# Optimization experiments

Measured on AMD Instinct MI355X. Metric: run time of the kernel, lower is better.

The kernel has to match this reference:

```python
import jax, jax.numpy as jnp
import numpy as np
from jax import lax

B, N, S, C_IN, C_OUT = 4, 16384, 4096, 256, 256


def setup_inputs() -> dict:
    key = jax.random.key(0)
    k1, k2, k3, k4 = jax.random.split(key, 4)
    xyz1 = jax.random.normal(k1, (B, 3, N), dtype=jnp.float32)
    xyz2 = jax.random.normal(k2, (B, 3, S), dtype=jnp.float32)
    points2 = jax.random.normal(k3, (B, C_IN, S), dtype=jnp.float32)
    W = jax.random.normal(k4, (C_OUT, C_IN), dtype=jnp.float32) * (1.0 / np.sqrt(C_IN))
    b = jnp.zeros((C_OUT,), dtype=jnp.float32)
    return {"xyz1": xyz1, "xyz2": xyz2, "points2": points2, "W": W, "b": b}


def reference(xyz1, xyz2, points2, W, b):
    # channel-first -> channel-last
    p1 = jnp.transpose(xyz1, (0, 2, 1))        # [B, N, 3]
    p2 = jnp.transpose(xyz2, (0, 2, 1))        # [B, S, 3]
    f2 = jnp.transpose(points2, (0, 2, 1))     # [B, S, C]
    Bn, Nn, _ = p1.shape
    Cn = f2.shape[-1]
    # squared pairwise distances [B, N, S]
    d = (-2.0 * jnp.einsum('bnc,bsc->bns', p1, p2)
         + jnp.sum(p1 * p1, axis=-1)[:, :, None]
         + jnp.sum(p2 * p2, axis=-1)[:, None, :])
    # 3 nearest neighbors (smallest distances) -- equivalent to sort + slice :3
    neg_d3, idx = lax.top_k(-d, 3)             # [B, N, 3]
    d3 = -neg_d3
    recip = 1.0 / (d3 + 1e-8)
    weight = recip / jnp.sum(recip, axis=-1, keepdims=True)   # [B, N, 3]
    # gather neighbor features: [B, N, 3, C]
    gathered = jnp.take_along_axis(
        f2, idx.reshape(Bn, Nn * 3)[..., None], axis=1
    ).reshape(Bn, Nn, 3, Cn)
    interp = jnp.sum(gathered * weight[..., None], axis=2)    # [B, N, C]
    # Conv1d(kernel=1) == per-point linear: [B, C_out, N]
    out = jnp.einsum('bnc,oc->bon', interp, W) + b[None, :, None]
    return out
```

## Files before the change

### kernel.cpp

```cpp
#include <hip/hip_runtime.h>

#define BB 4
#define NN 16384
#define SS 4096
#define CIN 256
#define COUT 256

#define SC 8
#define SCS (SS / SC)
#define KNNB ((NN / 512) * SC * BB)
#define GEMMB ((COUT / 64) * (SS / 64) * BB)

__device__ __forceinline__ unsigned short f2bf(float f) {
    unsigned u = __float_as_uint(f);
    u += 0x7FFF + ((u >> 16) & 1);
    return (unsigned short)(u >> 16);
}
__device__ __forceinline__ float bf2f(unsigned short h) {
    return __uint_as_float((unsigned)h << 16);
}

__global__ __launch_bounds__(256) void k_fused(const float* __restrict__ xyz1,
                                               const float* __restrict__ xyz2,
                                               const float* __restrict__ P,
                                               const float* __restrict__ W,
                                               const float* __restrict__ bias,
                                               unsigned short* __restrict__ Gh,
                                               float* __restrict__ pd,
                                               int* __restrict__ pi) {
    __shared__ float smem[2112];
    int bid = blockIdx.x;
    int t   = threadIdx.x;

    if (bid < KNNB) {
        int nb = bid & 31;
        int ch = (bid >> 5) & 7;
        int b  = bid >> 8;
        int s0 = ch * SCS;

        float4* smv = (float4*)smem;
        const float* x2 = xyz2 + (size_t)b * 3 * SS;
        for (int i = t; i < SCS; i += 256) {
            float px = x2[s0 + i];
            float py = x2[SS + s0 + i];
            float pz = x2[2 * SS + s0 + i];
            smv[i] = make_float4(px, py, pz, fmaf(px, px, fmaf(py, py, pz * pz)));
        }
        __syncthreads();

        int n0  = nb * 512 + t;
        int n1q = n0 + 256;
        const float* xb = xyz1 + (size_t)b * 3 * NN;
        float ax = xb[n0],  ay = xb[NN + n0],  az = xb[2 * NN + n0];
        float bx = xb[n1q], by = xb[NN + n1q], bz = xb[2 * NN + n1q];
        float an1 = fmaf(ax, ax, fmaf(ay, ay, az * az));
        float bn1 = fmaf(bx, bx, fmaf(by, by, bz * bz));
        float axm2 = -2.0f * ax, aym2 = -2.0f * ay, azm2 = -2.0f * az;
        float bxm2 = -2.0f * bx, bym2 = -2.0f * by, bzm2 = -2.0f * bz;

        float Ad0 = 3.4e38f, Ad1 = 3.4e38f, Ad2 = 3.4e38f;
        float Bd0 = 3.4e38f, Bd1 = 3.4e38f, Bd2 = 3.4e38f;
        int Ai0 = 0, Ai1 = 0, Ai2 = 0;
        int Bi0 = 0, Bi1 = 0, Bi2 = 0;

#pragma unroll 8
        for (int s = 0; s < SCS; ++s) {
            float4 p = smv[s];
            int gs = s0 + s;
            {
                float d = fmaf(p.x, axm2, fmaf(p.y, aym2,
                          fmaf(p.z, azm2, p.w + an1)));
                bool c0 = d < Ad0, c1 = d < Ad1, c2 = d < Ad2;
                Ad2 = __builtin_amdgcn_fmed3f(Ad1, d, Ad2);
                Ad1 = __builtin_amdgcn_fmed3f(Ad0, d, Ad1);
                Ad0 = fminf(Ad0, d);
                Ai2 = c1 ? Ai1 : (c2 ? gs : Ai2);
                Ai1 = c0 ? Ai0 : (c1 ? gs : Ai1);
                Ai0 = c0 ? gs : Ai0;
            }
            {
                float d = fmaf(p.x, bxm2, fmaf(p.y, bym2,
                          fmaf(p.z, bzm2, p.w + bn1)));
                bool c0 = d < Bd0, c1 = d < Bd1, c2 = d < Bd2;
                Bd2 = __builtin_amdgcn_fmed3f(Bd1, d, Bd2);
                Bd1 = __builtin_amdgcn_fmed3f(Bd0, d, Bd1);
                Bd0 = fminf(Bd0, d);
                Bi2 = c1 ? Bi1 : (c2 ? gs : Bi2);
                Bi1 = c0 ? Bi0 : (c1 ? gs : Bi1);
                Bi0 = c0 ? gs : Bi0;
            }
        }

        size_t cb = (size_t)(ch * BB + b) * 3;
        pd[(cb + 0) * NN + n0]  = Ad0;  pd[(cb + 1) * NN + n0]  = Ad1;
        pd[(cb + 2) * NN + n0]  = Ad2;
        pi[(cb + 0) * NN + n0]  = Ai0;  pi[(cb + 1) * NN + n0]  = Ai1;
        pi[(cb + 2) * NN + n0]  = Ai2;
        pd[(cb + 0) * NN + n1q] = Bd0;  pd[(cb + 1) * NN + n1q] = Bd1;
        pd[(cb + 2) * NN + n1q] = Bd2;
        pi[(cb + 0) * NN + n1q] = Bi0;  pi[(cb + 1) * NN + n1q] = Bi1;
        pi[(cb + 2) * NN + n1q] = Bi2;
    } else {
        int g  = bid - KNNB;
        int o0 = (g & 3) * 64;
        int s0 = ((g >> 2) & 63) * 64;
        int b  = g >> 8;
        float* sP = smem;
        float* sW = smem + 1024;
        int i = t & 15;
        int j = t >> 4;

        float acc[4][4];
#pragma unroll
        for (int p = 0; p < 4; ++p)
#pragma unroll
            for (int q = 0; q < 4; ++q) acc[p][q] = 0.f;

        const float* Pb = P + (size_t)b * CIN * SS;

        for (int c0 = 0; c0 < CIN; c0 += 16) {
            __syncthreads();
            {
                int col = t & 63;
                int r0r = t >> 6;
#pragma unroll
                for (int r = 0; r < 4; ++r) {
                    int row = r0r + r * 4;
                    sP[row * 64 + col] = Pb[(size_t)(c0 + row) * SS + s0 + col];
                }
            }
            {
                int cc = t & 15;
                int obase = t >> 4;
#pragma unroll
                for (int r = 0; r < 4; ++r) {
                    int oo = obase + 16 * r;
                    sW[cc * 68 + oo] = W[(size_t)(o0 + oo) * CIN + c0 + cc];
                }
            }
            __syncthreads();

#pragma unroll
            for (int cc = 0; cc < 16; ++cc) {
                float4 a  = *(const float4*)&sP[cc * 64 + i * 4];
                float4 bv = *(const float4*)&sW[cc * 68 + j * 4];
                float av[4] = {a.x, a.y, a.z, a.w};
                float bw[4] = {bv.x, bv.y, bv.z, bv.w};
#pragma unroll
                for (int p = 0; p < 4; ++p)
#pragma unroll
                    for (int q = 0; q < 4; ++q)
                        acc[p][q] = fmaf(av[p], bw[q], acc[p][q]);
            }
        }

        float b0 = bias[o0 + j * 4 + 0];
        float b1 = bias[o0 + j * 4 + 1];
        float b2 = bias[o0 + j * 4 + 2];
        float b3 = bias[o0 + j * 4 + 3];
#pragma unroll
        for (int p = 0; p < 4; ++p) {
            ushort4 v;
            v.x = f2bf(acc[p][0] + b0);
            v.y = f2bf(acc[p][1] + b1);
            v.z = f2bf(acc[p][2] + b2);
            v.w = f2bf(acc[p][3] + b3);
            size_t off = ((size_t)b * SS + s0 + i * 4 + p) * COUT + o0 + j * 4;
            *(ushort4*)&Gh[off] = v;
        }
    }
}

__global__ __launch_bounds__(256) void k_out(const unsigned short* __restrict__ Gh,
                                             const float* __restrict__ pd,
                                             const int* __restrict__ pi,
                                             float* __restrict__ out) {
    __shared__ float tile[64 * 65];
    __shared__ float ptd[64][12];
    __shared__ int   pti[64][12];
    __shared__ float sw[64][3];
    __shared__ int   si[64][3];
    int b    = blockIdx.y;
    int n0   = blockIdx.x * 64;
    int t    = threadIdx.x;
    int wave = t >> 6;
    int lane = t & 63;

    {
        int n = n0 + lane;
        float d0 = 3.4e38f, d1 = 3.4e38f, d2 = 3.4e38f;
        int i0 = 0, i1 = 0, i2 = 0;
#pragma unroll
        for (int c = 0; c < 2; ++c) {
            size_t cb = (size_t)((wave * 2 + c) * BB + b) * 3;
#pragma unroll
            for (int j = 0; j < 3; ++j) {
                float d = pd[(cb + j) * NN + n];
                int   s = pi[(cb + j) * NN + n];
                bool c0 = d < d0, c1 = d < d1, c2 = d < d2;
                d2 = __builtin_amdgcn_fmed3f(d1, d, d2);
                d1 = __builtin_amdgcn_fmed3f(d0, d, d1);
                d0 = fminf(d0, d);
                i2 = c1 ? i1 : (c2 ? s : i2);
                i1 = c0 ? i0 : (c1 ? s : i1);
                i0 = c0 ? s : i0;
            }
        }
        ptd[lane][wave * 3 + 0] = d0; pti[lane][wave * 3 + 0] = i0;
        ptd[lane][wave * 3 + 1] = d1; pti[lane][wave * 3 + 1] = i1;
        ptd[lane][wave * 3 + 2] = d2; pti[lane][wave * 3 + 2] = i2;
    }
    __syncthreads();
    if (t < 64) {
        float d0 = 3.4e38f, d1 = 3.4e38f, d2 = 3.4e38f;
        int i0 = 0, i1 = 0, i2 = 0;
#pragma unroll
        for (int c = 0; c < 12; ++c) {
            float d = ptd[t][c];
            int   s = pti[t][c];
            bool c0 = d < d0, c1 = d < d1, c2 = d < d2;
            d2 = __builtin_amdgcn_fmed3f(d1, d, d2);
            d1 = __builtin_amdgcn_fmed3f(d0, d, d1);
            d0 = fminf(d0, d);
            i2 = c1 ? i1 : (c2 ? s : i2);
            i1 = c0 ? i0 : (c1 ? s : i1);
            i0 = c0 ? s : i0;
        }
        float r0 = 1.0f / (d0 + 1e-8f);
        float r1 = 1.0f / (d1 + 1e-8f);
        float r2 = 1.0f / (d2 + 1e-8f);
        float inv = 1.0f / (r0 + r1 + r2);
        sw[t][0] = r0 * inv; sw[t][1] = r1 * inv; sw[t][2] = r2 * inv;
        si[t][0] = i0;       si[t][1] = i1;       si[t][2] = i2;
    }
    __syncthreads();

    const unsigned short* Gb = Gh + (size_t)b * SS * COUT;
    float* obase = out + (size_t)b * COUT * NN + n0 + lane;

    for (int oc = 0; oc < 4; ++oc) {
        int o0 = oc * 64;
#pragma unroll 4
        for (int qi = wave; qi < 64; qi += 4) {
            float w0 = sw[qi][0], w1 = sw[qi][1], w2 = sw[qi][2];
            const unsigned short* r0 = Gb + (size_t)si[qi][0] * COUT + o0;
            const unsigned short* r1 = Gb + (size_t)si[qi][1] * COUT + o0;
            const unsigned short* r2 = Gb + (size_t)si[qi][2] * COUT + o0;
            tile[qi * 65 + lane] = fmaf(w0, bf2f(r0[lane]),
                                   fmaf(w1, bf2f(r1[lane]),
                                        w2 * bf2f(r2[lane])));
        }
        __syncthreads();
#pragma unroll
        for (int j = 0; j < 16; ++j) {
            int c = wave * 16 + j;
            obase[(size_t)(o0 + c) * NN] = tile[lane * 65 + c];
        }
        __syncthreads();
    }
}

extern "C" void kernel_launch(void* const* d_in, const int* in_sizes, int n_in,
                              void* d_out, int out_size, void* d_ws, size_t ws_size,
                              hipStream_t stream) {
    const float* xyz1    = (const float*)d_in[0];
    const float* xyz2    = (const float*)d_in[1];
    const float* points2 = (const float*)d_in[2];
    const float* W       = (const float*)d_in[3];
    const float* bias    = (const float*)d_in[4];
    float* out = (float*)d_out;

    char* ws = (char*)d_ws;
    float*          pd = (float*)(ws);
    int*            pi = (int*)(ws + 6291456);
    unsigned short* Gh = (unsigned short*)(ws + 12582912);

    k_fused<<<dim3(KNNB + GEMMB), 256, 0, stream>>>(xyz1, xyz2, points2, W, bias,
                                                    Gh, pd, pi);
    k_out<<<dim3(NN / 64, BB), 256, 0, stream>>>(Gh, pd, pi, out);
}
```

Before: 226.9 us.

## Split top-3 merge into own kernel, vectorize and parallelize gather-output over channels

The per-query norm term is dropped from the inner distance loop and added only when the partial results are stored, removing one add per candidate. The chunk merge and weight computation move into a separate k_merge kernel that writes packed float4 weights and int4 indices. k_out now launches one block per 64-channel slice, so there are four times as many blocks. Each block gathers ushort4 vectors, so fewer, wider loads replace many scalar loads. This trades an extra launch and some workspace traffic for a shorter KNN inner loop and more parallel, vectorized gather/transpose work.

```diff
diff --git a/kernel.cpp b/kernel.cpp
--- a/kernel.cpp
+++ b/kernel.cpp
@@ -68,23 +68,21 @@
             float4 p = smv[s];
             int gs = s0 + s;
             {
-                float d = fmaf(p.x, axm2, fmaf(p.y, aym2,
-                          fmaf(p.z, azm2, p.w + an1)));
-                bool c0 = d < Ad0, c1 = d < Ad1, c2 = d < Ad2;
-                Ad2 = __builtin_amdgcn_fmed3f(Ad1, d, Ad2);
-                Ad1 = __builtin_amdgcn_fmed3f(Ad0, d, Ad1);
-                Ad0 = fminf(Ad0, d);
+                float e = fmaf(p.x, axm2, fmaf(p.y, aym2, fmaf(p.z, azm2, p.w)));
+                bool c0 = e < Ad0, c1 = e < Ad1, c2 = e < Ad2;
+                Ad2 = __builtin_amdgcn_fmed3f(Ad1, e, Ad2);
+                Ad1 = __builtin_amdgcn_fmed3f(Ad0, e, Ad1);
+                Ad0 = fminf(Ad0, e);
                 Ai2 = c1 ? Ai1 : (c2 ? gs : Ai2);
                 Ai1 = c0 ? Ai0 : (c1 ? gs : Ai1);
                 Ai0 = c0 ? gs : Ai0;
             }
             {
-                float d = fmaf(p.x, bxm2, fmaf(p.y, bym2,
-                          fmaf(p.z, bzm2, p.w + bn1)));
-                bool c0 = d < Bd0, c1 = d < Bd1, c2 = d < Bd2;
-                Bd2 = __builtin_amdgcn_fmed3f(Bd1, d, Bd2);
-                Bd1 = __builtin_amdgcn_fmed3f(Bd0, d, Bd1);
-                Bd0 = fminf(Bd0, d);
+                float e = fmaf(p.x, bxm2, fmaf(p.y, bym2, fmaf(p.z, bzm2, p.w)));
+                bool c0 = e < Bd0, c1 = e < Bd1, c2 = e < Bd2;
+                Bd2 = __builtin_amdgcn_fmed3f(Bd1, e, Bd2);
+                Bd1 = __builtin_amdgcn_fmed3f(Bd0, e, Bd1);
+                Bd0 = fminf(Bd0, e);
                 Bi2 = c1 ? Bi1 : (c2 ? gs : Bi2);
                 Bi1 = c0 ? Bi0 : (c1 ? gs : Bi1);
                 Bi0 = c0 ? gs : Bi0;
@@ -92,12 +90,12 @@
         }
 
         size_t cb = (size_t)(ch * BB + b) * 3;
-        pd[(cb + 0) * NN + n0]  = Ad0;  pd[(cb + 1) * NN + n0]  = Ad1;
-        pd[(cb + 2) * NN + n0]  = Ad2;
+        pd[(cb + 0) * NN + n0]  = Ad0 + an1;  pd[(cb + 1) * NN + n0]  = Ad1 + an1;
+        pd[(cb + 2) * NN + n0]  = Ad2 + an1;
         pi[(cb + 0) * NN + n0]  = Ai0;  pi[(cb + 1) * NN + n0]  = Ai1;
         pi[(cb + 2) * NN + n0]  = Ai2;
-        pd[(cb + 0) * NN + n1q] = Bd0;  pd[(cb + 1) * NN + n1q] = Bd1;
-        pd[(cb + 2) * NN + n1q] = Bd2;
+        pd[(cb + 0) * NN + n1q] = Bd0 + bn1;  pd[(cb + 1) * NN + n1q] = Bd1 + bn1;
+        pd[(cb + 2) * NN + n1q] = Bd2 + bn1;
         pi[(cb + 0) * NN + n1q] = Bi0;  pi[(cb + 1) * NN + n1q] = Bi1;
         pi[(cb + 2) * NN + n1q] = Bi2;
     } else {
@@ -171,53 +169,22 @@
     }
 }
 
-__global__ __launch_bounds__(256) void k_out(const unsigned short* __restrict__ Gh,
-                                             const float* __restrict__ pd,
-                                             const int* __restrict__ pi,
-                                             float* __restrict__ out) {
-    __shared__ float tile[64 * 65];
-    __shared__ float ptd[64][12];
-    __shared__ int   pti[64][12];
-    __shared__ float sw[64][3];
-    __shared__ int   si[64][3];
-    int b    = blockIdx.y;
-    int n0   = blockIdx.x * 64;
-    int t    = threadIdx.x;
-    int wave = t >> 6;
-    int lane = t & 63;
-
-    {
-        int n = n0 + lane;
-        float d0 = 3.4e38f, d1 = 3.4e38f, d2 = 3.4e38f;
-        int i0 = 0, i1 = 0, i2 = 0;
-#pragma unroll
-        for (int c = 0; c < 2; ++c) {
-            size_t cb = (size_t)((wave * 2 + c) * BB + b) * 3;
-#pragma unroll
-            for (int j = 0; j < 3; ++j) {
-                float d = pd[(cb + j) * NN + n];
-                int   s = pi[(cb + j) * NN + n];
-                bool c0 = d < d0, c1 = d < d1, c2 = d < d2;
-                d2 = __builtin_amdgcn_fmed3f(d1, d, d2);
-                d1 = __builtin_amdgcn_fmed3f(d0, d, d1);
-                d0 = fminf(d0, d);
-                i2 = c1 ? i1 : (c2 ? s : i2);
-                i1 = c0 ? i0 : (c1 ? s : i1);
-                i0 = c0 ? s : i0;
-            }
-        }
-        ptd[lane][wave * 3 + 0] = d0; pti[lane][wave * 3 + 0] = i0;
-        ptd[lane][wave * 3 + 1] = d1; pti[lane][wave * 3 + 1] = i1;
-        ptd[lane][wave * 3 + 2] = d2; pti[lane][wave * 3 + 2] = i2;
-    }
-    __syncthreads();
-    if (t < 64) {
-        float d0 = 3.4e38f, d1 = 3.4e38f, d2 = 3.4e38f;
-        int i0 = 0, i1 = 0, i2 = 0;
-#pragma unroll
-        for (int c = 0; c < 12; ++c) {
-            float d = ptd[t][c];
-            int   s = pti[t][c];
+__global__ __launch_bounds__(256) void k_merge(const float* __restrict__ pd,
+                                               const int* __restrict__ pi,
+                                               float4* __restrict__ wi4,
+                                               int4* __restrict__ gi4) {
+    int b = blockIdx.y;
+    int n = blockIdx.x * 256 + threadIdx.x;
+
+    float d0 = 3.4e38f, d1 = 3.4e38f, d2 = 3.4e38f;
+    int i0 = 0, i1 = 0, i2 = 0;
+#pragma unroll
+    for (int ch = 0; ch < SC; ++ch) {
+        size_t cb = (size_t)(ch * BB + b) * 3;
+#pragma unroll
+        for (int j = 0; j < 3; ++j) {
+            float d = pd[(cb + j) * NN + n];
+            int   s = pi[(cb + j) * NN + n];
             bool c0 = d < d0, c1 = d < d1, c2 = d < d2;
             d2 = __builtin_amdgcn_fmed3f(d1, d, d2);
             d1 = __builtin_amdgcn_fmed3f(d0, d, d1);
@@ -226,37 +193,70 @@
             i1 = c0 ? i0 : (c1 ? s : i1);
             i0 = c0 ? s : i0;
         }
-        float r0 = 1.0f / (d0 + 1e-8f);
-        float r1 = 1.0f / (d1 + 1e-8f);
-        float r2 = 1.0f / (d2 + 1e-8f);
-        float inv = 1.0f / (r0 + r1 + r2);
-        sw[t][0] = r0 * inv; sw[t][1] = r1 * inv; sw[t][2] = r2 * inv;
-        si[t][0] = i0;       si[t][1] = i1;       si[t][2] = i2;
+    }
+
+    float r0 = 1.0f / (d0 + 1e-8f);
+    float r1 = 1.0f / (d1 + 1e-8f);
+    float r2 = 1.0f / (d2 + 1e-8f);
+    float inv = 1.0f / (r0 + r1 + r2);
+    size_t q = (size_t)b * NN + n;
+    wi4[q] = make_float4(r0 * inv, r1 * inv, r2 * inv, 0.f);
+    gi4[q] = make_int4(i0, i1, i2, 0);
+}
+
+__global__ __launch_bounds__(256) void k_out(const unsigned short* __restrict__ Gh,
+                                             const float4* __restrict__ wi4,
+                                             const int4* __restrict__ gi4,
+                                             float* __restrict__ out) {
+    __shared__ float  tile[64 * 68];
+    __shared__ float4 swv[64];
+    __shared__ int4   siv[64];
+    int b    = blockIdx.z;
+    int oc   = blockIdx.y;
+    int n0   = blockIdx.x * 64;
+    int o0   = oc * 64;
+    int t    = threadIdx.x;
+    int wave = t >> 6;
+    int lane = t & 63;
+    int qg   = lane >> 4;
+    int c16  = lane & 15;
+
+    if (t < 64) {
+        size_t q = (size_t)b * NN + n0 + t;
+        swv[t] = wi4[q];
+        siv[t] = gi4[q];
     }
     __syncthreads();
 
     const unsigned short* Gb = Gh + (size_t)b * SS * COUT;
-    float* obase = out + (size_t)b * COUT * NN + n0 + lane;
-
-    for (int oc = 0; oc < 4; ++oc) {
-        int o0 = oc * 64;
-#pragma unroll 4
-        for (int qi = wave; qi < 64; qi += 4) {
-            float w0 = sw[qi][0], w1 = sw[qi][1], w2 = sw[qi][2];
-            const unsigned short* r0 = Gb + (size_t)si[qi][0] * COUT + o0;
-            const unsigned short* r1 = Gb + (size_t)si[qi][1] * COUT + o0;
-            const unsigned short* r2 = Gb + (size_t)si[qi][2] * COUT + o0;
-            tile[qi * 65 + lane] = fmaf(w0, bf2f(r0[lane]),
-                                   fmaf(w1, bf2f(r1[lane]),
-                                        w2 * bf2f(r2[lane])));
-        }
-        __syncthreads();
-#pragma unroll
-        for (int j = 0; j < 16; ++j) {
-            int c = wave * 16 + j;
-            obase[(size_t)(o0 + c) * NN] = tile[lane * 65 + c];
-        }
-        __syncthreads();
+
+#pragma unroll
+    for (int pass = 0; pass < 4; ++pass) {
+        int q = pass * 16 + wave * 4 + qg;
+        float4 wv = swv[q];
+        int4   iv = siv[q];
+        int co = o0 + c16 * 4;
+        ushort4 a0 = *(const ushort4*)(Gb + (size_t)iv.x * COUT + co);
+        ushort4 a1 = *(const ushort4*)(Gb + (size_t)iv.y * COUT + co);
+        ushort4 a2 = *(const ushort4*)(Gb + (size_t)iv.z * COUT + co);
+        float4 v;
+        v.x = fmaf(wv.x, bf2f(a0.x), fmaf(wv.y, bf2f(a1.x), wv.z * bf2f(a2.x)));
+        v.y = fmaf(wv.x, bf2f(a0.y), fmaf(wv.y, bf2f(a1.y), wv.z * bf2f(a2.y)));
+        v.z = fmaf(wv.x, bf2f(a0.z), fmaf(wv.y, bf2f(a1.z), wv.z * bf2f(a2.z)));
+        v.w = fmaf(wv.x, bf2f(a0.w), fmaf(wv.y, bf2f(a1.w), wv.z * bf2f(a2.w)));
+        *(float4*)&tile[q * 68 + c16 * 4] = v;
+    }
+    __syncthreads();
+
+    float* obase = out + ((size_t)b * COUT + o0) * NN + n0 + lane;
+#pragma unroll
+    for (int g = 0; g < 4; ++g) {
+        int c = wave * 16 + g * 4;
+        float4 v = *(const float4*)&tile[lane * 68 + c];
+        obase[(size_t)(c + 0) * NN] = v.x;
+        obase[(size_t)(c + 1) * NN] = v.y;
+        obase[(size_t)(c + 2) * NN] = v.z;
+        obase[(size_t)(c + 3) * NN] = v.w;
     }
 }
 
@@ -271,11 +271,14 @@
     float* out = (float*)d_out;
 
     char* ws = (char*)d_ws;
-    float*          pd = (float*)(ws);
-    int*            pi = (int*)(ws + 6291456);
-    unsigned short* Gh = (unsigned short*)(ws + 12582912);
+    float*          pd  = (float*)(ws);
+    int*            pi  = (int*)(ws + 6291456);
+    unsigned short* Gh  = (unsigned short*)(ws + 12582912);
+    float4*         wi4 = (float4*)(ws + 20971520);
+    int4*           gi4 = (int4*)(ws + 22020096);
 
     k_fused<<<dim3(KNNB + GEMMB), 256, 0, stream>>>(xyz1, xyz2, points2, W, bias,
                                                     Gh, pd, pi);
-    k_out<<<dim3(NN / 64, BB), 256, 0, stream>>>(Gh, pd, pi, out);
-}
+    k_merge<<<dim3(NN / 256, BB), 256, 0, stream>>>(pd, pi, wi4, gi4);
+    k_out<<<dim3(NN / 64, 4, BB), 256, 0, stream>>>(Gh, wi4, gi4, out);
+}
```

After: 224.5 us. About the same (-1.0%).
